# Optimization experiments

Hardware: AMD Instinct MI355X
Metric: run time of the kernel (lower is better)

Reference implementation:

```python
import jax, jax.numpy as jnp
import numpy as np


def _l2norm(x):
    # matches torch F.normalize(p=2, dim=-1) with eps clamp
    return x / jnp.clip(jnp.linalg.norm(x, axis=-1, keepdims=True), 1e-12)


def setup_inputs() -> dict:
    key = jax.random.key(0)
    k1, k2 = jax.random.split(key)
    I, J, S, H = 32, 32, 256, 768
    return {
        "query_embs": jax.random.normal(k1, (I, S, H), dtype=jnp.float32),
        "key_embs": jax.random.normal(k2, (J, S, H), dtype=jnp.float32),
        "q_mask": jnp.ones((I, S), dtype=jnp.float32),
        "k_mask": jnp.ones((J, S), dtype=jnp.float32),
        "alpha_raw": jnp.asarray(0.5, dtype=jnp.float32),  # learned scalar param
    }


def reference(query_embs, key_embs, q_mask, k_mask, alpha_raw):
    # eval path: gumbel_temp=None, use_max=False, do_distance=True, exp_decay=True
    S = query_embs.shape[1]
    pos = jnp.arange(S)
    distance = jnp.abs(pos[:, None] - pos[None, :]).astype(jnp.float32)  # [S, S]
    alpha = jax.nn.softplus(alpha_raw)

    qn = _l2norm(query_embs)  # [I, S, H]
    kn = _l2norm(key_embs)    # [J, T, H]

    # cross similarity [I, J, S, T] with exponential distance decay
    sim = jnp.einsum('ish,jth->ijst', qn, kn) * jnp.exp(-alpha * distance)

    # valid pair mask [I, J, S, T]
    valid = q_mask[:, None, :, None] * k_mask[None, :, None, :]
    masked = sim * valid - (1.0 - valid) * 1e9

    p = jax.nn.softmax(masked, axis=-1)             # softmax over key tokens t
    agg = jnp.einsum('ijst,jth->ijsh', p, kn)       # soft-aligned key embedding
    scores = jnp.einsum('ish,ijsh->ijs', qn, agg)   # per-query-token score
    scores = scores * q_mask[:, None, :]
    denom = jnp.clip(jnp.sum(q_mask, axis=-1, keepdims=True), 1.0)  # [I, 1]
    return jnp.sum(scores, axis=-1) / denom         # [I, J]
```

## Files before the change

### kernel.cpp

```cpp
#include <hip/hip_runtime.h>

#define I_DIM 32
#define J_DIM 32
#define S_DIM 256
#define H_DIM 768
#define KC    32
#define NCH   (H_DIM / KC)
#define QTILE_B 16384
#define KTILE_B 32768
#define WSQ_BYTES (I_DIM * 2 * NCH * QTILE_B)
#define WSK_BYTES (J_DIM * NCH * KTILE_B)
#define DTAB_OFF  (WSQ_BYTES + WSK_BYTES)

typedef _Float16 f16x8 __attribute__((ext_vector_type(8)));
typedef float    f32x16 __attribute__((ext_vector_type(16)));

static __device__ __forceinline__ unsigned short f16bits(_Float16 h) {
    union { _Float16 f; unsigned short u; } cv; cv.f = h; return cv.u;
}

__global__ __launch_bounds__(192) void li_split_kernel(
    const float* __restrict__ qe, const float* __restrict__ ke,
    char* __restrict__ wsQ, char* __restrict__ wsK)
{
    const int b = blockIdx.x;
    const int t = threadIdx.x;
    const bool isQ = b < I_DIM * S_DIM;
    const int row = isQ ? b : b - I_DIM * S_DIM;
    const float* base = (isQ ? qe : ke) + (size_t)row * H_DIM;

    const float4 v = *(const float4*)(base + 4 * t);
    float ss = v.x * v.x + v.y * v.y + v.z * v.z + v.w * v.w;
    #pragma unroll
    for (int m = 1; m < 64; m <<= 1) ss += __shfl_xor(ss, m, 64);
    __shared__ float red3[3];
    if ((t & 63) == 0) red3[t >> 6] = ss;
    __syncthreads();
    const float inv = 1.0f / fmaxf(sqrtf(red3[0] + red3[1] + red3[2]), 1e-12f);

    float xn[4] = {v.x * inv, v.y * inv, v.z * inv, v.w * inv};
    unsigned short hb[4], lb[4];
    #pragma unroll
    for (int e = 0; e < 4; ++e) {
        _Float16 h = (_Float16)xn[e];
        _Float16 lo = (_Float16)(xn[e] - (float)h);
        hb[e] = f16bits(h);
        lb[e] = f16bits(lo);
    }
    const unsigned int h01 = hb[0] | ((unsigned int)hb[1] << 16);
    const unsigned int h23 = hb[2] | ((unsigned int)hb[3] << 16);
    const unsigned int l01 = lb[0] | ((unsigned int)lb[1] << 16);
    const unsigned int l23 = lb[2] | ((unsigned int)lb[3] << 16);

    const int mi = row >> 8;
    const int s  = row & 255;
    const int k0 = 4 * t;
    const int c  = k0 >> 5;
    const int kk = k0 & 31;

    char* tile; int rr;
    if (isQ) { tile = wsQ + (size_t)((mi * 2 + (s >> 7)) * NCH + c) * QTILE_B; rr = s & 127; }
    else     { tile = wsK + (size_t)(mi * NCH + c) * KTILE_B;                  rr = s; }

    const int sh  = ((kk >> 3) ^ (rr & 7)) << 4;
    const int sl  = (((kk >> 3) | 4) ^ (rr & 7)) << 4;
    const int off = (kk & 7) * 2;
    *(uint2*)(tile + rr * 128 + sh + off) = make_uint2(h01, h23);
    *(uint2*)(tile + rr * 128 + sl + off) = make_uint2(l01, l23);
}

__global__ void li_dtab_kernel(const float* __restrict__ alpha_raw,
                               float* __restrict__ dtab)
{
    const float x = alpha_raw[0];
    const float alpha = (x > 20.0f) ? x : log1pf(expf(x));
    dtab[threadIdx.x] = expf(-alpha * (float)threadIdx.x);
}

__global__ __launch_bounds__(256, 2) void li_mfma_kernel(
    const char* __restrict__ wsQ, const char* __restrict__ wsK,
    const float* __restrict__ qm, const float* __restrict__ km,
    const float* __restrict__ dtab, float* __restrict__ out)
{
    __shared__ __align__(16) char sQ[QTILE_B];
    __shared__ __align__(16) char sK[KTILE_B];
    __shared__ float dsh[256], kmsh[256], qmsh[256], redA[256], redB[256];

    const int tid = threadIdx.x;
    const int wid = tid >> 6;
    const int l   = tid & 63;
    const int l31 = l & 31;
    const int hi  = l >> 5;

    const int bidx = blockIdx.x;
    const int x  = bidx & 7;
    const int r0 = bidx >> 3;
    const int j  = x * 4 + (r0 & 3);
    const int i  = r0 >> 2;

    dsh[tid]  = dtab[tid];
    kmsh[tid] = km[j * 256 + tid];
    qmsh[tid] = qm[i * 256 + tid];
    __syncthreads();

    float total = 0.0f;

    for (int st = 0; st < 2; ++st) {
        f32x16 acc[8];
        #pragma unroll
        for (int nt = 0; nt < 8; ++nt)
            #pragma unroll
            for (int z = 0; z < 16; ++z) acc[nt][z] = 0.0f;

        for (int c = 0; c < NCH; ++c) {
            const char* qt = wsQ + (size_t)((i * 2 + st) * NCH + c) * QTILE_B;
            const char* kt = wsK + (size_t)(j * NCH + c) * KTILE_B;
            #pragma unroll
            for (int u = 0; u < 4; ++u)
                __builtin_amdgcn_global_load_lds(
                    (const __attribute__((address_space(1))) void*)(qt + wid * 4096 + u * 1024 + l * 16),
                    (__attribute__((address_space(3))) void*)(sQ + wid * 4096 + u * 1024), 16, 0, 0);
            #pragma unroll
            for (int u = 0; u < 8; ++u)
                __builtin_amdgcn_global_load_lds(
                    (const __attribute__((address_space(1))) void*)(kt + wid * 8192 + u * 1024 + l * 16),
                    (__attribute__((address_space(3))) void*)(sK + wid * 8192 + u * 1024), 16, 0, 0);
            __syncthreads();

            #pragma unroll
            for (int ks = 0; ks < 2; ++ks) {
                const int kkb = ks * 16 + hi * 8;
                const int r7  = l31 & 7;
                const int sH  = (((kkb >> 3)) ^ r7) << 4;
                const int sL  = (((kkb >> 3) | 4) ^ r7) << 4;
                const int rq  = wid * 32 + l31;
                const f16x8 qh = *(const f16x8*)(sQ + rq * 128 + sH);
                const f16x8 ql = *(const f16x8*)(sQ + rq * 128 + sL);
                #pragma unroll
                for (int nt = 0; nt < 8; ++nt) {
                    const int rk = nt * 32 + l31;
                    const f16x8 kh = *(const f16x8*)(sK + rk * 128 + sH);
                    const f16x8 kl = *(const f16x8*)(sK + rk * 128 + sL);
                    acc[nt] = __builtin_amdgcn_mfma_f32_32x32x16_f16(qh, kh, acc[nt], 0, 0, 0);
                    acc[nt] = __builtin_amdgcn_mfma_f32_32x32x16_f16(qh, kl, acc[nt], 0, 0, 0);
                    acc[nt] = __builtin_amdgcn_mfma_f32_32x32x16_f16(ql, kh, acc[nt], 0, 0, 0);
                }
            }
            __syncthreads();
        }

        #pragma unroll
        for (int reg = 0; reg < 16; ++reg) {
            const int srow = st * 128 + wid * 32 + hi * 4 + (reg & 3) + 8 * (reg >> 2);
            const float qms = qmsh[srow];
            float mv[8], cvv[8];
            float mloc = -3.0e38f;
            #pragma unroll
            for (int nt = 0; nt < 8; ++nt) {
                const int tcol = nt * 32 + l31;
                const float cv = acc[nt][reg];
                int dd = srow - tcol; dd = dd < 0 ? -dd : dd;
                const float valid = qms * kmsh[tcol];
                const float m = cv * dsh[dd] * valid - (1.0f - valid) * 1e9f;
                mv[nt] = m; cvv[nt] = cv;
                mloc = fmaxf(mloc, m);
            }
            #pragma unroll
            for (int mm = 1; mm < 32; mm <<= 1)
                mloc = fmaxf(mloc, __shfl_xor(mloc, mm, 32));
            float L = 0.0f, W = 0.0f;
            #pragma unroll
            for (int nt = 0; nt < 8; ++nt) {
                const float e = __expf(mv[nt] - mloc);
                L += e;
                W += e * cvv[nt];
            }
            #pragma unroll
            for (int mm = 1; mm < 32; mm <<= 1) {
                L += __shfl_xor(L, mm, 32);
                W += __shfl_xor(W, mm, 32);
            }
            if (l31 == 0) total += (W / L) * qms;
        }
    }

    redA[tid] = total;
    redB[tid] = qmsh[tid];
    __syncthreads();
    for (int off = 128; off > 0; off >>= 1) {
        if (tid < off) {
            redA[tid] += redA[tid + off];
            redB[tid] += redB[tid + off];
        }
        __syncthreads();
    }
    if (tid == 0) out[i * 32 + j] = redA[0] / fmaxf(redB[0], 1.0f);
}

extern "C" void kernel_launch(void* const* d_in, const int* in_sizes, int n_in,
                              void* d_out, int out_size, void* d_ws, size_t ws_size,
                              hipStream_t stream)
{
    const float* qe = (const float*)d_in[0];
    const float* ke = (const float*)d_in[1];
    const float* qm = (const float*)d_in[2];
    const float* km = (const float*)d_in[3];
    const float* al = (const float*)d_in[4];
    float* out = (float*)d_out;

    char* ws   = (char*)d_ws;
    char* wsQ  = ws;
    char* wsK  = ws + WSQ_BYTES;
    float* dtab = (float*)(ws + DTAB_OFF);

    hipLaunchKernelGGL(li_split_kernel, dim3((I_DIM + J_DIM) * S_DIM), dim3(192),
                       0, stream, qe, ke, wsQ, wsK);
    hipLaunchKernelGGL(li_dtab_kernel, dim3(1), dim3(256), 0, stream, al, dtab);
    hipLaunchKernelGGL(li_mfma_kernel, dim3(I_DIM * J_DIM), dim3(256), 0, stream,
                       wsQ, wsK, qm, km, dtab, out);
}
```

Measured before the change: 422.8 us.

## Compute full 256x256 tile per block with 8 waves, double-buffered LDS, split softmax

The MFMA kernel now has 512 threads (8 waves in a 2x4 grid) and computes the whole 256x256 similarity tile at once, so the key tiles are no longer loaded twice per (i,j) pair. The next H-chunk is staged into double-buffered LDS while the current one is being computed. The softmax is split across the two column halves and merged with a max-rescaled combine in shared memory. The dtab kernel is removed and the decay is computed inline with __expf. The split kernel now normalizes one row per wave with no block sync. Doubling LDS to 128KB plus larger register use may cut occupancy.

```diff
diff --git a/kernel.cpp b/kernel.cpp
--- a/kernel.cpp
+++ b/kernel.cpp
@@ -6,11 +6,9 @@
 #define H_DIM 768
 #define KC    32
 #define NCH   (H_DIM / KC)
-#define QTILE_B 16384
-#define KTILE_B 32768
-#define WSQ_BYTES (I_DIM * 2 * NCH * QTILE_B)
-#define WSK_BYTES (J_DIM * NCH * KTILE_B)
-#define DTAB_OFF  (WSQ_BYTES + WSK_BYTES)
+#define TILE_B 32768
+#define WSQ_BYTES ((size_t)I_DIM * NCH * TILE_B)
+#define WSK_BYTES ((size_t)J_DIM * NCH * TILE_B)
 
 typedef _Float16 f16x8 __attribute__((ext_vector_type(8)));
 typedef float    f32x16 __attribute__((ext_vector_type(16)));
@@ -19,78 +17,73 @@
     union { _Float16 f; unsigned short u; } cv; cv.f = h; return cv.u;
 }
 
-__global__ __launch_bounds__(192) void li_split_kernel(
+__global__ __launch_bounds__(256) void li_split_kernel(
     const float* __restrict__ qe, const float* __restrict__ ke,
     char* __restrict__ wsQ, char* __restrict__ wsK)
 {
-    const int b = blockIdx.x;
-    const int t = threadIdx.x;
-    const bool isQ = b < I_DIM * S_DIM;
-    const int row = isQ ? b : b - I_DIM * S_DIM;
+    const int lane = threadIdx.x & 63;
+    const int w    = threadIdx.x >> 6;
+    const int r    = blockIdx.x * 4 + w;
+    const bool isQ = r < I_DIM * S_DIM;
+    const int row  = isQ ? r : r - I_DIM * S_DIM;
     const float* base = (isQ ? qe : ke) + (size_t)row * H_DIM;
 
-    const float4 v = *(const float4*)(base + 4 * t);
-    float ss = v.x * v.x + v.y * v.y + v.z * v.z + v.w * v.w;
+    float4 v[3];
+    v[0] = *(const float4*)(base + 4 * lane);
+    v[1] = *(const float4*)(base + 4 * lane + 256);
+    v[2] = *(const float4*)(base + 4 * lane + 512);
+    float ss = 0.0f;
+    #pragma unroll
+    for (int g = 0; g < 3; ++g)
+        ss += v[g].x * v[g].x + v[g].y * v[g].y + v[g].z * v[g].z + v[g].w * v[g].w;
     #pragma unroll
     for (int m = 1; m < 64; m <<= 1) ss += __shfl_xor(ss, m, 64);
-    __shared__ float red3[3];
-    if ((t & 63) == 0) red3[t >> 6] = ss;
-    __syncthreads();
-    const float inv = 1.0f / fmaxf(sqrtf(red3[0] + red3[1] + red3[2]), 1e-12f);
-
-    float xn[4] = {v.x * inv, v.y * inv, v.z * inv, v.w * inv};
-    unsigned short hb[4], lb[4];
-    #pragma unroll
-    for (int e = 0; e < 4; ++e) {
-        _Float16 h = (_Float16)xn[e];
-        _Float16 lo = (_Float16)(xn[e] - (float)h);
-        hb[e] = f16bits(h);
-        lb[e] = f16bits(lo);
-    }
-    const unsigned int h01 = hb[0] | ((unsigned int)hb[1] << 16);
-    const unsigned int h23 = hb[2] | ((unsigned int)hb[3] << 16);
-    const unsigned int l01 = lb[0] | ((unsigned int)lb[1] << 16);
-    const unsigned int l23 = lb[2] | ((unsigned int)lb[3] << 16);
-
-    const int mi = row >> 8;
-    const int s  = row & 255;
-    const int k0 = 4 * t;
-    const int c  = k0 >> 5;
-    const int kk = k0 & 31;
-
-    char* tile; int rr;
-    if (isQ) { tile = wsQ + (size_t)((mi * 2 + (s >> 7)) * NCH + c) * QTILE_B; rr = s & 127; }
-    else     { tile = wsK + (size_t)(mi * NCH + c) * KTILE_B;                  rr = s; }
-
-    const int sh  = ((kk >> 3) ^ (rr & 7)) << 4;
-    const int sl  = (((kk >> 3) | 4) ^ (rr & 7)) << 4;
-    const int off = (kk & 7) * 2;
-    *(uint2*)(tile + rr * 128 + sh + off) = make_uint2(h01, h23);
-    *(uint2*)(tile + rr * 128 + sl + off) = make_uint2(l01, l23);
-}
-
-__global__ void li_dtab_kernel(const float* __restrict__ alpha_raw,
-                               float* __restrict__ dtab)
-{
-    const float x = alpha_raw[0];
-    const float alpha = (x > 20.0f) ? x : log1pf(expf(x));
-    dtab[threadIdx.x] = expf(-alpha * (float)threadIdx.x);
-}
-
-__global__ __launch_bounds__(256, 2) void li_mfma_kernel(
+    const float inv = 1.0f / fmaxf(sqrtf(ss), 1e-12f);
+
+    const int mi  = row >> 8;
+    const int s   = row & 255;
+    const int r7  = s & 7;
+    char* wsb = (isQ ? wsQ : wsK) + (size_t)mi * NCH * TILE_B + s * 128;
+
+    #pragma unroll
+    for (int g = 0; g < 3; ++g) {
+        const int k0 = 4 * lane + 256 * g;
+        const int c  = k0 >> 5;
+        const int kk = k0 & 31;
+        float xn[4] = {v[g].x * inv, v[g].y * inv, v[g].z * inv, v[g].w * inv};
+        unsigned short hb[4], lb[4];
+        #pragma unroll
+        for (int e = 0; e < 4; ++e) {
+            _Float16 h  = (_Float16)xn[e];
+            _Float16 lo = (_Float16)(xn[e] - (float)h);
+            hb[e] = f16bits(h);
+            lb[e] = f16bits(lo);
+        }
+        char* p = wsb + (size_t)c * TILE_B + (((kk >> 3) ^ r7) << 4) + (kk & 7) * 2;
+        *(uint2*)(p)        = make_uint2(hb[0] | ((unsigned)hb[1] << 16), hb[2] | ((unsigned)hb[3] << 16));
+        *(uint2*)((char*)((size_t)p ^ 64)) = make_uint2(lb[0] | ((unsigned)lb[1] << 16), lb[2] | ((unsigned)lb[3] << 16));
+    }
+}
+
+__global__ __launch_bounds__(512, 2) void li_mfma_kernel(
     const char* __restrict__ wsQ, const char* __restrict__ wsK,
     const float* __restrict__ qm, const float* __restrict__ km,
-    const float* __restrict__ dtab, float* __restrict__ out)
+    const float* __restrict__ alpha_raw, float* __restrict__ out)
 {
-    __shared__ __align__(16) char sQ[QTILE_B];
-    __shared__ __align__(16) char sK[KTILE_B];
-    __shared__ float dsh[256], kmsh[256], qmsh[256], redA[256], redB[256];
+    __shared__ __align__(16) char sQ[2][TILE_B];
+    __shared__ __align__(16) char sK[2][TILE_B];
+    __shared__ float kmsh[256], qmsh[256];
+    __shared__ float pm[256][2], pL[256][2], pW[256][2];
+    __shared__ float redA[512], redB[512];
 
     const int tid = threadIdx.x;
     const int wid = tid >> 6;
     const int l   = tid & 63;
     const int l31 = l & 31;
     const int hi  = l >> 5;
+    const int wx  = wid & 1;
+    const int wy  = wid >> 1;
+    const int r7  = l31 & 7;
 
     const int bidx = blockIdx.x;
     const int x  = bidx & 7;
@@ -98,70 +91,101 @@
     const int j  = x * 4 + (r0 & 3);
     const int i  = r0 >> 2;
 
-    dsh[tid]  = dtab[tid];
-    kmsh[tid] = km[j * 256 + tid];
-    qmsh[tid] = qm[i * 256 + tid];
+    if (tid < 256) {
+        kmsh[tid] = km[j * 256 + tid];
+        qmsh[tid] = qm[i * 256 + tid];
+    }
+    const float araw  = alpha_raw[0];
+    const float alpha = (araw > 20.0f) ? araw : log1pf(expf(araw));
+    const float nal   = -alpha;
+
+    const char* qbase = wsQ + (size_t)i * NCH * TILE_B;
+    const char* kbase = wsK + (size_t)j * NCH * TILE_B;
+
+    f32x16 acc[2][4];
+    #pragma unroll
+    for (int mr = 0; mr < 2; ++mr)
+        #pragma unroll
+        for (int nt = 0; nt < 4; ++nt)
+            #pragma unroll
+            for (int z = 0; z < 16; ++z) acc[mr][nt][z] = 0.0f;
+
+#define STAGE(buf, c)                                                                      \
+    do {                                                                                   \
+        const char* qt_ = qbase + (size_t)(c) * TILE_B + wid * 4096 + l * 16;              \
+        const char* kt_ = kbase + (size_t)(c) * TILE_B + wid * 4096 + l * 16;              \
+        char* dq_ = sQ[buf] + wid * 4096;                                                  \
+        char* dk_ = sK[buf] + wid * 4096;                                                  \
+        _Pragma("unroll")                                                                  \
+        for (int u = 0; u < 4; ++u)                                                        \
+            __builtin_amdgcn_global_load_lds(                                              \
+                (const __attribute__((address_space(1))) void*)(qt_ + u * 1024),           \
+                (__attribute__((address_space(3))) void*)(dq_ + u * 1024), 16, 0, 0);      \
+        _Pragma("unroll")                                                                  \
+        for (int u = 0; u < 4; ++u)                                                        \
+            __builtin_amdgcn_global_load_lds(                                              \
+                (const __attribute__((address_space(1))) void*)(kt_ + u * 1024),           \
+                (__attribute__((address_space(3))) void*)(dk_ + u * 1024), 16, 0, 0);      \
+    } while (0)
+
+    STAGE(0, 0);
     __syncthreads();
 
-    float total = 0.0f;
-
-    for (int st = 0; st < 2; ++st) {
-        f32x16 acc[8];
-        #pragma unroll
-        for (int nt = 0; nt < 8; ++nt)
-            #pragma unroll
-            for (int z = 0; z < 16; ++z) acc[nt][z] = 0.0f;
-
-        for (int c = 0; c < NCH; ++c) {
-            const char* qt = wsQ + (size_t)((i * 2 + st) * NCH + c) * QTILE_B;
-            const char* kt = wsK + (size_t)(j * NCH + c) * KTILE_B;
-            #pragma unroll
-            for (int u = 0; u < 4; ++u)
-                __builtin_amdgcn_global_load_lds(
-                    (const __attribute__((address_space(1))) void*)(qt + wid * 4096 + u * 1024 + l * 16),
-                    (__attribute__((address_space(3))) void*)(sQ + wid * 4096 + u * 1024), 16, 0, 0);
-            #pragma unroll
-            for (int u = 0; u < 8; ++u)
-                __builtin_amdgcn_global_load_lds(
-                    (const __attribute__((address_space(1))) void*)(kt + wid * 8192 + u * 1024 + l * 16),
-                    (__attribute__((address_space(3))) void*)(sK + wid * 8192 + u * 1024), 16, 0, 0);
-            __syncthreads();
-
-            #pragma unroll
-            for (int ks = 0; ks < 2; ++ks) {
-                const int kkb = ks * 16 + hi * 8;
-                const int r7  = l31 & 7;
-                const int sH  = (((kkb >> 3)) ^ r7) << 4;
-                const int sL  = (((kkb >> 3) | 4) ^ r7) << 4;
-                const int rq  = wid * 32 + l31;
-                const f16x8 qh = *(const f16x8*)(sQ + rq * 128 + sH);
-                const f16x8 ql = *(const f16x8*)(sQ + rq * 128 + sL);
-                #pragma unroll
-                for (int nt = 0; nt < 8; ++nt) {
-                    const int rk = nt * 32 + l31;
-                    const f16x8 kh = *(const f16x8*)(sK + rk * 128 + sH);
-                    const f16x8 kl = *(const f16x8*)(sK + rk * 128 + sL);
-                    acc[nt] = __builtin_amdgcn_mfma_f32_32x32x16_f16(qh, kh, acc[nt], 0, 0, 0);
-                    acc[nt] = __builtin_amdgcn_mfma_f32_32x32x16_f16(qh, kl, acc[nt], 0, 0, 0);
-                    acc[nt] = __builtin_amdgcn_mfma_f32_32x32x16_f16(ql, kh, acc[nt], 0, 0, 0);
-                }
-            }
-            __syncthreads();
-        }
-
+    for (int c = 0; c < NCH; ++c) {
+        if (c + 1 < NCH) STAGE((c + 1) & 1, c + 1);
+        const char* bQ = sQ[c & 1];
+        const char* bK = sK[c & 1];
+        #pragma unroll
+        for (int ks = 0; ks < 2; ++ks) {
+            const int soff = ((ks * 2 + hi) ^ r7) << 4;
+            const int rA = wy * 64 + l31;
+            const int rB = rA + 32;
+            const f16x8 qhA = *(const f16x8*)(bQ + rA * 128 + soff);
+            const f16x8 qlA = *(const f16x8*)(bQ + ((rA * 128 + soff) ^ 64));
+            const f16x8 qhB = *(const f16x8*)(bQ + rB * 128 + soff);
+            const f16x8 qlB = *(const f16x8*)(bQ + ((rB * 128 + soff) ^ 64));
+            f16x8 kh[4], kl[4];
+            #pragma unroll
+            for (int nt = 0; nt < 4; ++nt) {
+                const int rk = wx * 128 + nt * 32 + l31;
+                kh[nt] = *(const f16x8*)(bK + rk * 128 + soff);
+                kl[nt] = *(const f16x8*)(bK + ((rk * 128 + soff) ^ 64));
+            }
+            #pragma unroll
+            for (int nt = 0; nt < 4; ++nt) {
+                acc[0][nt] = __builtin_amdgcn_mfma_f32_32x32x16_f16(qhA, kh[nt], acc[0][nt], 0, 0, 0);
+                acc[1][nt] = __builtin_amdgcn_mfma_f32_32x32x16_f16(qhB, kh[nt], acc[1][nt], 0, 0, 0);
+            }
+            #pragma unroll
+            for (int nt = 0; nt < 4; ++nt) {
+                acc[0][nt] = __builtin_amdgcn_mfma_f32_32x32x16_f16(qhA, kl[nt], acc[0][nt], 0, 0, 0);
+                acc[1][nt] = __builtin_amdgcn_mfma_f32_32x32x16_f16(qhB, kl[nt], acc[1][nt], 0, 0, 0);
+            }
+            #pragma unroll
+            for (int nt = 0; nt < 4; ++nt) {
+                acc[0][nt] = __builtin_amdgcn_mfma_f32_32x32x16_f16(qlA, kh[nt], acc[0][nt], 0, 0, 0);
+                acc[1][nt] = __builtin_amdgcn_mfma_f32_32x32x16_f16(qlB, kh[nt], acc[1][nt], 0, 0, 0);
+            }
+        }
+        __syncthreads();
+    }
+#undef STAGE
+
+    #pragma unroll
+    for (int mrep = 0; mrep < 2; ++mrep) {
         #pragma unroll
         for (int reg = 0; reg < 16; ++reg) {
-            const int srow = st * 128 + wid * 32 + hi * 4 + (reg & 3) + 8 * (reg >> 2);
+            const int srow = wy * 64 + mrep * 32 + hi * 4 + (reg & 3) + 8 * (reg >> 2);
             const float qms = qmsh[srow];
-            float mv[8], cvv[8];
+            float mv[4], cvv[4];
             float mloc = -3.0e38f;
             #pragma unroll
-            for (int nt = 0; nt < 8; ++nt) {
-                const int tcol = nt * 32 + l31;
-                const float cv = acc[nt][reg];
+            for (int nt = 0; nt < 4; ++nt) {
+                const int tcol = wx * 128 + nt * 32 + l31;
+                const float cv = acc[mrep][nt][reg];
                 int dd = srow - tcol; dd = dd < 0 ? -dd : dd;
                 const float valid = qms * kmsh[tcol];
-                const float m = cv * dsh[dd] * valid - (1.0f - valid) * 1e9f;
+                const float m = cv * __expf(nal * (float)dd) * valid - (1.0f - valid) * 1e9f;
                 mv[nt] = m; cvv[nt] = cv;
                 mloc = fmaxf(mloc, m);
             }
@@ -170,7 +194,7 @@
                 mloc = fmaxf(mloc, __shfl_xor(mloc, mm, 32));
             float L = 0.0f, W = 0.0f;
             #pragma unroll
-            for (int nt = 0; nt < 8; ++nt) {
+            for (int nt = 0; nt < 4; ++nt) {
                 const float e = __expf(mv[nt] - mloc);
                 L += e;
                 W += e * cvv[nt];
@@ -180,14 +204,29 @@
                 L += __shfl_xor(L, mm, 32);
                 W += __shfl_xor(W, mm, 32);
             }
-            if (l31 == 0) total += (W / L) * qms;
-        }
-    }
-
-    redA[tid] = total;
-    redB[tid] = qmsh[tid];
+            if (l31 == 0) {
+                pm[srow][wx] = mloc;
+                pL[srow][wx] = L;
+                pW[srow][wx] = W;
+            }
+        }
+    }
     __syncthreads();
-    for (int off = 128; off > 0; off >>= 1) {
+
+    float contrib = 0.0f, qq = 0.0f;
+    if (tid < 256) {
+        const float m0 = pm[tid][0], m1 = pm[tid][1];
+        const float M  = fmaxf(m0, m1);
+        const float e0 = __expf(m0 - M), e1 = __expf(m1 - M);
+        const float L  = pL[tid][0] * e0 + pL[tid][1] * e1;
+        const float W  = pW[tid][0] * e0 + pW[tid][1] * e1;
+        contrib = (W / L) * qmsh[tid];
+        qq = qmsh[tid];
+    }
+    redA[tid] = contrib;
+    redB[tid] = qq;
+    __syncthreads();
+    for (int off = 256; off > 0; off >>= 1) {
         if (tid < off) {
             redA[tid] += redA[tid + off];
             redB[tid] += redB[tid + off];
@@ -208,14 +247,11 @@
     const float* al = (const float*)d_in[4];
     float* out = (float*)d_out;
 
-    char* ws   = (char*)d_ws;
-    char* wsQ  = ws;
-    char* wsK  = ws + WSQ_BYTES;
-    float* dtab = (float*)(ws + DTAB_OFF);
-
-    hipLaunchKernelGGL(li_split_kernel, dim3((I_DIM + J_DIM) * S_DIM), dim3(192),
+    char* wsQ = (char*)d_ws;
+    char* wsK = wsQ + WSQ_BYTES;
+
+    hipLaunchKernelGGL(li_split_kernel, dim3((I_DIM + J_DIM) * S_DIM / 4), dim3(256),
                        0, stream, qe, ke, wsQ, wsK);
-    hipLaunchKernelGGL(li_dtab_kernel, dim3(1), dim3(256), 0, stream, al, dtab);
-    hipLaunchKernelGGL(li_mfma_kernel, dim3(I_DIM * J_DIM), dim3(256), 0, stream,
-                       wsQ, wsK, qm, km, dtab, out);
-}
+    hipLaunchKernelGGL(li_mfma_kernel, dim3(I_DIM * J_DIM), dim3(512), 0, stream,
+                       wsQ, wsK, qm, km, al, out);
+}
```

After: 416.3 us. Within noise of the previous version (-1.6%).
